# Optimization experiments

Measured on AMD Instinct MI355X. Metric: run time of the kernel, lower is better.

Reference implementation:

```python
import jax, jax.numpy as jnp
import numpy as np

B, C_IN, N, T = 16, 2, 207, 12
E = 1863
EMB = 64
HEADS = 8
F_DIM = EMB * T  # 768


def setup_inputs() -> dict:
    key = jax.random.key(0)
    ks = jax.random.split(key, 12)
    s = 0.05
    x = jax.random.normal(ks[0], (B, C_IN, N, T), jnp.float32)
    src = jax.random.randint(ks[1], (E,), 0, N)
    dst = jax.random.randint(ks[2], (E,), 0, N)
    # ensure every node has an incoming edge (self loops in the tail)
    loop = jnp.arange(N)
    src = src.at[-N:].set(loop)
    dst = dst.at[-N:].set(loop)
    Ws = jax.random.normal(ks[3], (EMB, C_IN), jnp.float32) * s
    bs = jnp.zeros((EMB,), jnp.float32)
    Wc = jax.random.normal(ks[4], (EMB, C_IN), jnp.float32) * s
    bc = jnp.zeros((EMB,), jnp.float32)
    W1 = jax.random.normal(ks[5], (F_DIM, HEADS * F_DIM), jnp.float32) * s
    al1 = jax.random.normal(ks[6], (HEADS, F_DIM), jnp.float32) * s
    ar1 = jax.random.normal(ks[7], (HEADS, F_DIM), jnp.float32) * s
    b1 = jnp.zeros((HEADS, F_DIM), jnp.float32)
    W2 = jax.random.normal(ks[8], (F_DIM, HEADS * F_DIM), jnp.float32) * s
    al2 = jax.random.normal(ks[9], (HEADS, F_DIM), jnp.float32) * s
    ar2 = jax.random.normal(ks[10], (HEADS, F_DIM), jnp.float32) * s
    b2 = jnp.zeros((HEADS, F_DIM), jnp.float32)
    return dict(x=x, src=src, dst=dst, Ws=Ws, bs=bs, Wc=Wc, bc=bc,
                W1=W1, al1=al1, ar1=ar1, b1=b1, W2=W2, al2=al2, ar2=ar2, b2=b2)


def _gat_layer(h, W, al, ar, b, src, dst):
    # h: [B, N, F]  (dropout disabled: eval-mode reference)
    feat = (h @ W).reshape(B, N, HEADS, F_DIM)          # [B,N,H,F]
    el = jnp.einsum('bnhf,hf->bnh', feat, al)           # src scores
    er = jnp.einsum('bnhf,hf->bnh', feat, ar)           # dst scores
    e = jax.nn.leaky_relu(el[:, src] + er[:, dst], 0.2)  # [B,E,H]

    def edge_softmax(ev):  # ev: [E,H], softmax over edges sharing a dst node
        m = jax.ops.segment_max(ev, dst, num_segments=N)
        ex = jnp.exp(ev - m[dst])
        denom = jax.ops.segment_sum(ex, dst, num_segments=N)
        return ex / denom[dst]

    alpha = jax.vmap(edge_softmax)(e)                   # [B,E,H]
    msg = alpha[..., None] * feat[:, src]               # [B,E,H,F]
    rst = jax.vmap(lambda m_: jax.ops.segment_sum(m_, dst, num_segments=N))(msg)
    rst = jax.nn.elu(rst + b)                            # bias + F.elu activation
    return rst.mean(axis=2)                              # mean over heads -> [B,N,F]


def reference(x, src, dst, Ws, bs, Wc, bc, W1, al1, ar1, b1, W2, al2, ar2, b2):
    # 1x1 convs == channel matmuls
    x1 = jnp.einsum('bcnt,oc->bont', x, Ws) + bs[None, :, None, None]
    x2 = jax.nn.leaky_relu(jnp.einsum('bcnt,oc->bont', x, Wc) + bc[None, :, None, None], 0.01)
    xm = x1 + x2                                         # [B,EMB,N,T]
    h = xm.transpose(0, 2, 1, 3).reshape(B, N, F_DIM)    # [B,N,768]
    h = _gat_layer(h, W1, al1, ar1, b1, src, dst)
    h = _gat_layer(h, W2, al2, ar2, b2, src, dst)
    gc = h.reshape(B, N, EMB, T).transpose(0, 2, 1, 3)   # [B,EMB,N,T]
    return xm + gc
```

## Files before the change

### kernel.cpp

```cpp
#include <hip/hip_runtime.h>

#define BB 16
#define NNODE 207
#define TTS 12
#define NE 1863
#define NEP2 1920
#define NH 8
#define FD 768
#define HFD 6144
#define MM 3312
#define MP 3328

typedef short bf16x8 __attribute__((ext_vector_type(8)));
typedef float f32x4 __attribute__((ext_vector_type(4)));

typedef __attribute__((address_space(3))) unsigned int lds_u32;
typedef __attribute__((address_space(1))) const unsigned int glb_u32;

__device__ __forceinline__ unsigned short f2b(float f) {
    unsigned int u = __float_as_uint(f);
    u = (u + 0x7FFFu + ((u >> 16) & 1u)) >> 16;
    return (unsigned short)u;
}
__device__ __forceinline__ float b2f(unsigned short b) {
    return __uint_as_float(((unsigned int)b) << 16);
}

#define CSR_EBLK 468
__global__ __launch_bounds__(256) void prep_misc(const float* __restrict__ W1,
                                                 const float* __restrict__ al1, const float* __restrict__ ar1,
                                                 const float* __restrict__ W2,
                                                 const float* __restrict__ al2, const float* __restrict__ ar2,
                                                 float* __restrict__ wlr,
                                                 unsigned short* __restrict__ Wt1,
                                                 unsigned short* __restrict__ Wt2,
                                                 const int* __restrict__ dst,
                                                 int* __restrict__ ptr, int* __restrict__ cidx) {
    __shared__ __align__(16) char smem[16640];
    const int bid = blockIdx.x;
    const int t = threadIdx.x;
    const int wv = t >> 6, lane = t & 63;
    if (bid < 3072) {
        const int wid = bid * 4 + wv;
        const int which = wid / 6144;
        const int r = wid % 6144;
        const int k = r >> 3, hh = r & 7;
        const float* W = which ? W2 : W1;
        const float* al = which ? al2 : al1;
        const float* ar = which ? ar2 : ar1;
        const float4* wp = (const float4*)(W + (size_t)k * HFD + hh * FD);
        const float4* ap = (const float4*)(al + hh * FD);
        const float4* rp = (const float4*)(ar + hh * FD);
        float sl = 0.f, sr = 0.f;
#pragma unroll
        for (int jj = 0; jj < 3; jj++) {
            int j = lane + jj * 64;
            float4 w = wp[j], a = ap[j], b = rp[j];
            sl += w.x * a.x + w.y * a.y + w.z * a.z + w.w * a.w;
            sr += w.x * b.x + w.y * b.y + w.z * b.z + w.w * b.w;
        }
#pragma unroll
        for (int off = 32; off > 0; off >>= 1) {
            sl += __shfl_down(sl, off);
            sr += __shfl_down(sr, off);
        }
        if (lane == 0) {
            wlr[(size_t)which * 12288 + 0 + hh * FD + k] = sl;
            wlr[(size_t)which * 12288 + 6144 + hh * FD + k] = sr;
        }
    } else if (bid < 5376) {
        float (*tile)[65] = (float(*)[65])smem;
        const int idx = bid - 3072;
        const int which = idx / 1152;
        const int r2 = idx % 1152;
        const int k0 = (r2 % 12) * 64;
        const int n0 = (r2 / 12) * 64;
        const float* W = which ? W2 : W1;
        unsigned short* Wt = which ? Wt2 : Wt1;
        const int c = t & 63, r0 = t >> 6;
#pragma unroll
        for (int i = 0; i < 16; i++) {
            int r = r0 + i * 4;
            tile[r][c] = W[(size_t)(k0 + r) * HFD + n0 + c];
        }
        __syncthreads();
#pragma unroll
        for (int i = 0; i < 16; i++) {
            int r = r0 + i * 4;
            Wt[(size_t)(n0 + r) * FD + k0 + c] = f2b(tile[c][r]);
        }
    } else {
        int* dl = (int*)smem;
        const int b2 = bid - 5376;
        for (int i = t; i < NEP2; i += 256) dl[i] = (i < NE) ? dst[i] : 0x0FFFFFFF;
        __syncthreads();
        if (b2 < CSR_EBLK) {
            const int e = b2 * 4 + wv;
            if (e >= NE) return;
            const int d = dl[e];
            int pos = 0;
#pragma unroll
            for (int j = 0; j < 30; j++) {
                int i = lane + j * 64;
                int di = dl[i];
                pos += (int)(di < d) + (int)((i < e) & (di == d));
            }
#pragma unroll
            for (int off = 32; off > 0; off >>= 1) pos += __shfl_down(pos, off);
            if (lane == 0) cidx[pos] = e;
        } else {
            const int n = (b2 - CSR_EBLK) * 4 + wv;
            if (n > NNODE) return;
            int cnt = 0;
#pragma unroll
            for (int j = 0; j < 30; j++) cnt += (int)(dl[lane + j * 64] < n);
#pragma unroll
            for (int off = 32; off > 0; off >>= 1) cnt += __shfl_down(cnt, off);
            if (lane == 0) ptr[n] = cnt;
        }
    }
}

__global__ __launch_bounds__(256) void prep_h(const float* __restrict__ x,
                                              const float* __restrict__ Ws, const float* __restrict__ bs,
                                              const float* __restrict__ Wc, const float* __restrict__ bc,
                                              const float* __restrict__ wl, const float* __restrict__ wr,
                                              const int* __restrict__ src, const int* __restrict__ cidx,
                                              int* __restrict__ esrc,
                                              float* __restrict__ h0, unsigned short* __restrict__ hbf,
                                              float* __restrict__ el, float* __restrict__ er) {
    __shared__ float redl[4][8], redr[4][8];
    const int bn = blockIdx.x;
    const int t = threadIdx.x;
    if (bn >= MP) {
        int p = (bn - MP) * 256 + t;
        if (p < NE) esrc[p] = src[cidx[p]];
        return;
    }
    if (bn >= MM) {
#pragma unroll
        for (int c = 0; c < 3; c++) hbf[(size_t)bn * FD + c * 256 + t] = 0;
        return;
    }
    const int b = bn / NNODE, n = bn % NNODE;
    float pl[8] = {}, pr[8] = {};
#pragma unroll
    for (int c = 0; c < 3; c++) {
        int idx = c * 256 + t;
        int e = idx / TTS, tt = idx % TTS;
        float x0 = x[((size_t)(b * 2 + 0) * NNODE + n) * TTS + tt];
        float x1 = x[((size_t)(b * 2 + 1) * NNODE + n) * TTS + tt];
        float s1 = Ws[e * 2] * x0 + Ws[e * 2 + 1] * x1 + bs[e];
        float s2 = Wc[e * 2] * x0 + Wc[e * 2 + 1] * x1 + bc[e];
        s2 = s2 > 0.f ? s2 : 0.01f * s2;
        float v = s1 + s2;
        h0[(size_t)bn * FD + idx] = v;
        hbf[(size_t)bn * FD + idx] = f2b(v);
#pragma unroll
        for (int hh = 0; hh < 8; hh++) {
            pl[hh] += v * wl[hh * FD + idx];
            pr[hh] += v * wr[hh * FD + idx];
        }
    }
    const int wv = t >> 6, lane = t & 63;
#pragma unroll
    for (int hh = 0; hh < 8; hh++) {
        float a = pl[hh], c2 = pr[hh];
#pragma unroll
        for (int off = 32; off > 0; off >>= 1) {
            a += __shfl_down(a, off);
            c2 += __shfl_down(c2, off);
        }
        if (lane == 0) { redl[wv][hh] = a; redr[wv][hh] = c2; }
    }
    __syncthreads();
    if (t < 8) {
        el[bn * NH + t] = redl[0][t] + redl[1][t] + redl[2][t] + redl[3][t];
        er[bn * NH + t] = redr[0][t] + redr[1][t] + redr[2][t] + redr[3][t];
    }
}

__global__ __launch_bounds__(256) void gemm_bf16(const unsigned short* __restrict__ A,
                                                 const unsigned short* __restrict__ Bt,
                                                 unsigned short* __restrict__ C) {
    __shared__ __align__(16) unsigned short Alds[128 * 64];
    __shared__ __align__(16) unsigned short Blds[128 * 64];
    const int t = threadIdx.x;
    const int lane = t & 63;
    const int wv = t >> 6;
    const int wr = (wv >> 1) * 64, wc = (wv & 1) * 64;
    const int mt = blockIdx.y * 128, nt = blockIdx.x * 128;
    const int lm = lane & 15;
    const int s4 = lane >> 4;
    const int sl0 = ((0 + s4) ^ (lm & 7)) * 8;
    const int sl1 = ((4 + s4) ^ (lm & 7)) * 8;

    const int rr = lane >> 3;
    const int ssl = ((lane & 7) ^ rr) * 8;
    const unsigned short* ap[4];
    const unsigned short* bp[4];
#pragma unroll
    for (int q = 0; q < 4; q++) {
        int row = wv * 32 + q * 8 + rr;
        ap[q] = A + (size_t)(mt + row) * FD + ssl;
        bp[q] = Bt + (size_t)(nt + row) * FD + ssl;
    }

    f32x4 acc[4][4] = {};
    for (int ks = 0; ks < FD; ks += 64) {
#pragma unroll
        for (int q = 0; q < 4; q++) {
            __builtin_amdgcn_global_load_lds((glb_u32*)(ap[q] + ks),
                (lds_u32*)(Alds + (wv * 4 + q) * 512), 16, 0, 0);
            __builtin_amdgcn_global_load_lds((glb_u32*)(bp[q] + ks),
                (lds_u32*)(Blds + (wv * 4 + q) * 512), 16, 0, 0);
        }
        __syncthreads();
        {
            bf16x8 af[4], bfv[4];
#pragma unroll
            for (int i = 0; i < 4; i++)
                af[i] = *(const bf16x8*)(Alds + (wr + i * 16 + lm) * 64 + sl0);
#pragma unroll
            for (int j = 0; j < 4; j++)
                bfv[j] = *(const bf16x8*)(Blds + (wc + j * 16 + lm) * 64 + sl0);
#pragma unroll
            for (int i = 0; i < 4; i++)
#pragma unroll
                for (int j = 0; j < 4; j++)
                    acc[i][j] = __builtin_amdgcn_mfma_f32_16x16x32_bf16(af[i], bfv[j], acc[i][j], 0, 0, 0);
        }
        {
            bf16x8 af[4], bfv[4];
#pragma unroll
            for (int i = 0; i < 4; i++)
                af[i] = *(const bf16x8*)(Alds + (wr + i * 16 + lm) * 64 + sl1);
#pragma unroll
            for (int j = 0; j < 4; j++)
                bfv[j] = *(const bf16x8*)(Blds + (wc + j * 16 + lm) * 64 + sl1);
#pragma unroll
            for (int i = 0; i < 4; i++)
#pragma unroll
                for (int j = 0; j < 4; j++)
                    acc[i][j] = __builtin_amdgcn_mfma_f32_16x16x32_bf16(af[i], bfv[j], acc[i][j], 0, 0, 0);
        }
        __syncthreads();
    }
    const int rbase = s4 * 4;
#pragma unroll
    for (int i = 0; i < 4; i++) {
#pragma unroll
        for (int r = 0; r < 4; r++) {
            int grow = mt + wr + i * 16 + rbase + r;
            if (grow < MM) {
#pragma unroll
                for (int j = 0; j < 4; j++) {
                    int gcol = nt + wc + j * 16 + lm;
                    C[(size_t)grow * HFD + gcol] = f2b(acc[i][j][r]);
                }
            }
        }
    }
}

template <int LAST>
__global__ __launch_bounds__(512) void msg_agg(const unsigned short* __restrict__ feat,
                                               const int* __restrict__ cptr, const int* __restrict__ esrc,
                                               const float* __restrict__ bias,
                                               const float* __restrict__ el_in, const float* __restrict__ er_in,
                                               unsigned short* __restrict__ hbf_out,
                                               const float* __restrict__ wl, const float* __restrict__ wr,
                                               float* __restrict__ el_out, float* __restrict__ er_out,
                                               const float* __restrict__ h0, float* __restrict__ out) {
    __shared__ float rstl[HFD];
    __shared__ int src_l[64];
    __shared__ float alph[64][NH];
    __shared__ float redl[8][8], redr[8][8];
    __shared__ float sm_m[8], sm_i[8], sm_er[8];
    const int bn = (blockIdx.x & 7) * (MM / 8) + (blockIdx.x >> 3);
    const int b = bn / NNODE, n = bn % NNODE;
    const int t = threadIdx.x;
    const int p0 = cptr[n], p1 = cptr[n + 1];
    const int deg = p1 - p0;
    if (t < 64) {
        const int h = t & 7, js = t >> 3;
        const float erv = er_in[(b * NNODE + n) * NH + h];
        float m = -1e30f, d = 0.f;
        for (int jb = 0; jb < deg; jb += 8) {
            int j = jb + js;
            float s = -1e30f, add = 0.f;
            if (j < deg) {
                int sn = esrc[p0 + j];
                s = el_in[(b * NNODE + sn) * NH + h] + erv;
                s = s > 0.f ? s : 0.2f * s;
                add = 1.f;
            }
            float mn = fmaxf(m, s);
            d = d * __expf(m - mn) + add * __expf(s - mn);
            m = mn;
        }
#pragma unroll
        for (int o = 8; o < 64; o <<= 1) {
            float mo = __shfl_xor(m, o), dd = __shfl_xor(d, o);
            float mn = fmaxf(m, mo);
            d = d * __expf(m - mn) + dd * __expf(mo - mn);
            m = mn;
        }
        if (js == 0) { sm_m[h] = m; sm_i[h] = 1.f / d; sm_er[h] = erv; }
    }
    __syncthreads();

    const int hq0 = (0 * 512 + t) / 192;
    const int hq1 = (1 * 512 + t) / 192;
    const int hq2 = (2 * 512 + t) / 192;
    float acc[3][4] = {};
    for (int base = p0; base < p1; base += 64) {
        const int cnt = min(64, p1 - base);
        if (t < cnt) src_l[t] = esrc[base + t];
        {
            int j = t >> 3, hh = t & 7;
            if (j < cnt) {
                float s = el_in[(b * NNODE + esrc[base + j]) * NH + hh] + sm_er[hh];
                s = s > 0.f ? s : 0.2f * s;
                alph[j][hh] = __expf(s - sm_m[hh]) * sm_i[hh];
            }
        }
        __syncthreads();
        for (int j2 = 0; j2 < cnt; j2++) {
            const uint2* fp = (const uint2*)(feat + (size_t)(b * NNODE + src_l[j2]) * HFD);
            const float a0 = alph[j2][hq0], a1 = alph[j2][hq1], a2 = alph[j2][hq2];
            uint2 v0 = fp[0 * 512 + t], v1 = fp[1 * 512 + t], v2 = fp[2 * 512 + t];
            unsigned int w;
            w = v0.x; acc[0][0] += a0 * b2f((unsigned short)w); acc[0][1] += a0 * b2f((unsigned short)(w >> 16));
            w = v0.y; acc[0][2] += a0 * b2f((unsigned short)w); acc[0][3] += a0 * b2f((unsigned short)(w >> 16));
            w = v1.x; acc[1][0] += a1 * b2f((unsigned short)w); acc[1][1] += a1 * b2f((unsigned short)(w >> 16));
            w = v1.y; acc[1][2] += a1 * b2f((unsigned short)w); acc[1][3] += a1 * b2f((unsigned short)(w >> 16));
            w = v2.x; acc[2][0] += a2 * b2f((unsigned short)w); acc[2][1] += a2 * b2f((unsigned short)(w >> 16));
            w = v2.y; acc[2][2] += a2 * b2f((unsigned short)w); acc[2][3] += a2 * b2f((unsigned short)(w >> 16));
        }
        __syncthreads();
    }
#pragma unroll
    for (int q = 0; q < 3; q++) {
        int s = q * 512 + t;
#pragma unroll
        for (int u = 0; u < 4; u++) rstl[s * 4 + u] = acc[q][u];
    }
    __syncthreads();
    float pl[8] = {}, pr[8] = {};
#pragma unroll
    for (int q2 = 0; q2 < 2; q2++) {
        int f = q2 * 512 + t;
        if (f < FD) {
            float val = 0.f;
#pragma unroll
            for (int hh = 0; hh < 8; hh++) {
                float r = rstl[hh * FD + f] + bias[hh * FD + f];
                val += (r > 0.f) ? r : (expf(r) - 1.f);
            }
            val *= 0.125f;
            if (LAST) {
                int e_ = f / TTS, tt_ = f % TTS;
                out[((size_t)(b * 64 + e_) * NNODE + n) * TTS + tt_] = h0[(size_t)bn * FD + f] + val;
            } else {
                hbf_out[(size_t)bn * FD + f] = f2b(val);
#pragma unroll
                for (int hh = 0; hh < 8; hh++) {
                    pl[hh] += val * wl[hh * FD + f];
                    pr[hh] += val * wr[hh * FD + f];
                }
            }
        }
    }
    if (!LAST) {
        const int wv = t >> 6, lane = t & 63;
#pragma unroll
        for (int hh = 0; hh < 8; hh++) {
            float a = pl[hh], c2 = pr[hh];
#pragma unroll
            for (int off = 32; off > 0; off >>= 1) {
                a += __shfl_down(a, off);
                c2 += __shfl_down(c2, off);
            }
            if (lane == 0) { redl[wv][hh] = a; redr[wv][hh] = c2; }
        }
        __syncthreads();
        if (t < 8) {
            float a = 0.f, c2 = 0.f;
#pragma unroll
            for (int wv2 = 0; wv2 < 8; wv2++) { a += redl[wv2][t]; c2 += redr[wv2][t]; }
            el_out[bn * NH + t] = a;
            er_out[bn * NH + t] = c2;
        }
    }
}

extern "C" void kernel_launch(void* const* d_in, const int* in_sizes, int n_in,
                              void* d_out, int out_size, void* d_ws, size_t ws_size,
                              hipStream_t stream) {
    const float* x = (const float*)d_in[0];
    const int* src = (const int*)d_in[1];
    const int* dst = (const int*)d_in[2];
    const float* Ws = (const float*)d_in[3];
    const float* bs = (const float*)d_in[4];
    const float* Wc = (const float*)d_in[5];
    const float* bc = (const float*)d_in[6];
    const float* W1 = (const float*)d_in[7];
    const float* al1 = (const float*)d_in[8];
    const float* ar1 = (const float*)d_in[9];
    const float* b1 = (const float*)d_in[10];
    const float* W2 = (const float*)d_in[11];
    const float* al2 = (const float*)d_in[12];
    const float* ar2 = (const float*)d_in[13];
    const float* b2 = (const float*)d_in[14];
    float* out = (float*)d_out;

    char* w = (char*)d_ws;
    size_t off = 0;
    auto alloc = [&](size_t bytes) -> void* {
        void* p = w + off;
        off = (off + bytes + 255) & ~(size_t)255;
        return p;
    };
    float* h0 = (float*)alloc((size_t)MM * FD * 4);
    unsigned short* hbf = (unsigned short*)alloc((size_t)MP * FD * 2);
    unsigned short* Wt1 = (unsigned short*)alloc((size_t)HFD * FD * 2);
    unsigned short* Wt2 = (unsigned short*)alloc((size_t)HFD * FD * 2);
    unsigned short* feat = (unsigned short*)alloc((size_t)MM * HFD * 2);
    float* el = (float*)alloc((size_t)MM * NH * 4);
    float* er = (float*)alloc((size_t)MM * NH * 4);
    float* el2 = (float*)alloc((size_t)MM * NH * 4);
    float* er2 = (float*)alloc((size_t)MM * NH * 4);
    int* cptr = (int*)alloc((NNODE + 1) * 4);
    int* cidx = (int*)alloc(NE * 4);
    int* esrc = (int*)alloc(NE * 4);
    float* wlr = (float*)alloc((size_t)4 * 6144 * 4);
    float* wl1 = wlr, * wr1 = wlr + 6144, * wl2 = wlr + 12288, * wr2 = wlr + 18432;

    prep_misc<<<5896, 256, 0, stream>>>(W1, al1, ar1, W2, al2, ar2, wlr, Wt1, Wt2, dst, cptr, cidx);
    prep_h<<<MP + 8, 256, 0, stream>>>(x, Ws, bs, Wc, bc, wl1, wr1, src, cidx, esrc, h0, hbf, el, er);

    gemm_bf16<<<dim3(48, 26), 256, 0, stream>>>(hbf, Wt1, feat);
    msg_agg<0><<<MM, 512, 0, stream>>>(feat, cptr, esrc, b1, el, er, hbf, wl2, wr2, el2, er2, nullptr, nullptr);

    gemm_bf16<<<dim3(48, 26), 256, 0, stream>>>(hbf, Wt2, feat);
    msg_agg<1><<<MM, 512, 0, stream>>>(feat, cptr, esrc, b2, el2, er2, nullptr, nullptr, nullptr, nullptr, nullptr, h0, out);
}
```

Before: 215.1 us.

## Halve msg_agg block size, widen feature loads, prefetch next edge's row

The message-aggregation kernel now runs 256 threads per block instead of 512. Each thread loads 16-byte vectors, eight bf16 features at a time, and accumulates 3x8 values. While the current edge is being accumulated, the next edge's source feature row is loaded into registers, so gather latency overlaps with the FMAs. Edge chunks and the wave-reduction arrays shrink to match. In exchange, register pressure per thread rises and there are fewer threads per node to hide latency.

```diff
diff --git a/kernel.cpp b/kernel.cpp
--- a/kernel.cpp
+++ b/kernel.cpp
@@ -264,7 +264,7 @@
 }
 
 template <int LAST>
-__global__ __launch_bounds__(512) void msg_agg(const unsigned short* __restrict__ feat,
+__global__ __launch_bounds__(256) void msg_agg(const unsigned short* __restrict__ feat,
                                                const int* __restrict__ cptr, const int* __restrict__ esrc,
                                                const float* __restrict__ bias,
                                                const float* __restrict__ el_in, const float* __restrict__ er_in,
@@ -273,9 +273,9 @@
                                                float* __restrict__ el_out, float* __restrict__ er_out,
                                                const float* __restrict__ h0, float* __restrict__ out) {
     __shared__ float rstl[HFD];
-    __shared__ int src_l[64];
-    __shared__ float alph[64][NH];
-    __shared__ float redl[8][8], redr[8][8];
+    __shared__ int src_l[32];
+    __shared__ float alph[32][NH];
+    __shared__ float redl[4][8], redr[4][8];
     __shared__ float sm_m[8], sm_i[8], sm_er[8];
     const int bn = (blockIdx.x & 7) * (MM / 8) + (blockIdx.x >> 3);
     const int b = bn / NNODE, n = bn % NNODE;
@@ -310,12 +310,10 @@
     }
     __syncthreads();
 
-    const int hq0 = (0 * 512 + t) / 192;
-    const int hq1 = (1 * 512 + t) / 192;
-    const int hq2 = (2 * 512 + t) / 192;
-    float acc[3][4] = {};
-    for (int base = p0; base < p1; base += 64) {
-        const int cnt = min(64, p1 - base);
+    const int h0i = t / 96, h1i = (256 + t) / 96, h2i = (512 + t) / 96;
+    float acc[3][8] = {};
+    for (int base = p0; base < p1; base += 32) {
+        const int cnt = min(32, p1 - base);
         if (t < cnt) src_l[t] = esrc[base + t];
         {
             int j = t >> 3, hh = t & 7;
@@ -326,49 +324,63 @@
             }
         }
         __syncthreads();
+        const unsigned short* fp = feat + (size_t)(b * NNODE + src_l[0]) * HFD;
+        uint4 c0 = *(const uint4*)(fp + (size_t)(0 * 256 + t) * 8);
+        uint4 c1 = *(const uint4*)(fp + (size_t)(1 * 256 + t) * 8);
+        uint4 c2 = *(const uint4*)(fp + (size_t)(2 * 256 + t) * 8);
         for (int j2 = 0; j2 < cnt; j2++) {
-            const uint2* fp = (const uint2*)(feat + (size_t)(b * NNODE + src_l[j2]) * HFD);
-            const float a0 = alph[j2][hq0], a1 = alph[j2][hq1], a2 = alph[j2][hq2];
-            uint2 v0 = fp[0 * 512 + t], v1 = fp[1 * 512 + t], v2 = fp[2 * 512 + t];
+            uint4 n0, n1, n2;
+            if (j2 + 1 < cnt) {
+                const unsigned short* np = feat + (size_t)(b * NNODE + src_l[j2 + 1]) * HFD;
+                n0 = *(const uint4*)(np + (size_t)(0 * 256 + t) * 8);
+                n1 = *(const uint4*)(np + (size_t)(1 * 256 + t) * 8);
+                n2 = *(const uint4*)(np + (size_t)(2 * 256 + t) * 8);
+            }
+            const float a0 = alph[j2][h0i], a1 = alph[j2][h1i], a2 = alph[j2][h2i];
             unsigned int w;
-            w = v0.x; acc[0][0] += a0 * b2f((unsigned short)w); acc[0][1] += a0 * b2f((unsigned short)(w >> 16));
-            w = v0.y; acc[0][2] += a0 * b2f((unsigned short)w); acc[0][3] += a0 * b2f((unsigned short)(w >> 16));
-            w = v1.x; acc[1][0] += a1 * b2f((unsigned short)w); acc[1][1] += a1 * b2f((unsigned short)(w >> 16));
-            w = v1.y; acc[1][2] += a1 * b2f((unsigned short)w); acc[1][3] += a1 * b2f((unsigned short)(w >> 16));
-            w = v2.x; acc[2][0] += a2 * b2f((unsigned short)w); acc[2][1] += a2 * b2f((unsigned short)(w >> 16));
-            w = v2.y; acc[2][2] += a2 * b2f((unsigned short)w); acc[2][3] += a2 * b2f((unsigned short)(w >> 16));
-        }
-        __syncthreads();
-    }
-#pragma unroll
-    for (int q = 0; q < 3; q++) {
-        int s = q * 512 + t;
-#pragma unroll
-        for (int u = 0; u < 4; u++) rstl[s * 4 + u] = acc[q][u];
+            w = c0.x; acc[0][0] += a0 * b2f((unsigned short)w); acc[0][1] += a0 * b2f((unsigned short)(w >> 16));
+            w = c0.y; acc[0][2] += a0 * b2f((unsigned short)w); acc[0][3] += a0 * b2f((unsigned short)(w >> 16));
+            w = c0.z; acc[0][4] += a0 * b2f((unsigned short)w); acc[0][5] += a0 * b2f((unsigned short)(w >> 16));
+            w = c0.w; acc[0][6] += a0 * b2f((unsigned short)w); acc[0][7] += a0 * b2f((unsigned short)(w >> 16));
+            w = c1.x; acc[1][0] += a1 * b2f((unsigned short)w); acc[1][1] += a1 * b2f((unsigned short)(w >> 16));
+            w = c1.y; acc[1][2] += a1 * b2f((unsigned short)w); acc[1][3] += a1 * b2f((unsigned short)(w >> 16));
+            w = c1.z; acc[1][4] += a1 * b2f((unsigned short)w); acc[1][5] += a1 * b2f((unsigned short)(w >> 16));
+            w = c1.w; acc[1][6] += a1 * b2f((unsigned short)w); acc[1][7] += a1 * b2f((unsigned short)(w >> 16));
+            w = c2.x; acc[2][0] += a2 * b2f((unsigned short)w); acc[2][1] += a2 * b2f((unsigned short)(w >> 16));
+            w = c2.y; acc[2][2] += a2 * b2f((unsigned short)w); acc[2][3] += a2 * b2f((unsigned short)(w >> 16));
+            w = c2.z; acc[2][4] += a2 * b2f((unsigned short)w); acc[2][5] += a2 * b2f((unsigned short)(w >> 16));
+            w = c2.w; acc[2][6] += a2 * b2f((unsigned short)w); acc[2][7] += a2 * b2f((unsigned short)(w >> 16));
+            c0 = n0; c1 = n1; c2 = n2;
+        }
+        __syncthreads();
+    }
+#pragma unroll
+    for (int c = 0; c < 3; c++) {
+        int v = c * 256 + t;
+#pragma unroll
+        for (int u = 0; u < 8; u++) rstl[v * 8 + u] = acc[c][u];
     }
     __syncthreads();
     float pl[8] = {}, pr[8] = {};
 #pragma unroll
-    for (int q2 = 0; q2 < 2; q2++) {
-        int f = q2 * 512 + t;
-        if (f < FD) {
-            float val = 0.f;
+    for (int q = 0; q < 3; q++) {
+        int f = q * 256 + t;
+        float val = 0.f;
+#pragma unroll
+        for (int hh = 0; hh < 8; hh++) {
+            float r = rstl[hh * FD + f] + bias[hh * FD + f];
+            val += (r > 0.f) ? r : (expf(r) - 1.f);
+        }
+        val *= 0.125f;
+        if (LAST) {
+            int e_ = f / TTS, tt_ = f % TTS;
+            out[((size_t)(b * 64 + e_) * NNODE + n) * TTS + tt_] = h0[(size_t)bn * FD + f] + val;
+        } else {
+            hbf_out[(size_t)bn * FD + f] = f2b(val);
 #pragma unroll
             for (int hh = 0; hh < 8; hh++) {
-                float r = rstl[hh * FD + f] + bias[hh * FD + f];
-                val += (r > 0.f) ? r : (expf(r) - 1.f);
-            }
-            val *= 0.125f;
-            if (LAST) {
-                int e_ = f / TTS, tt_ = f % TTS;
-                out[((size_t)(b * 64 + e_) * NNODE + n) * TTS + tt_] = h0[(size_t)bn * FD + f] + val;
-            } else {
-                hbf_out[(size_t)bn * FD + f] = f2b(val);
-#pragma unroll
-                for (int hh = 0; hh < 8; hh++) {
-                    pl[hh] += val * wl[hh * FD + f];
-                    pr[hh] += val * wr[hh * FD + f];
-                }
+                pl[hh] += val * wl[hh * FD + f];
+                pr[hh] += val * wr[hh * FD + f];
             }
         }
     }
@@ -386,11 +398,8 @@
         }
         __syncthreads();
         if (t < 8) {
-            float a = 0.f, c2 = 0.f;
-#pragma unroll
-            for (int wv2 = 0; wv2 < 8; wv2++) { a += redl[wv2][t]; c2 += redr[wv2][t]; }
-            el_out[bn * NH + t] = a;
-            er_out[bn * NH + t] = c2;
+            el_out[bn * NH + t] = redl[0][t] + redl[1][t] + redl[2][t] + redl[3][t];
+            er_out[bn * NH + t] = redr[0][t] + redr[1][t] + redr[2][t] + redr[3][t];
         }
     }
 }
@@ -441,8 +450,8 @@
     prep_h<<<MP + 8, 256, 0, stream>>>(x, Ws, bs, Wc, bc, wl1, wr1, src, cidx, esrc, h0, hbf, el, er);
 
     gemm_bf16<<<dim3(48, 26), 256, 0, stream>>>(hbf, Wt1, feat);
-    msg_agg<0><<<MM, 512, 0, stream>>>(feat, cptr, esrc, b1, el, er, hbf, wl2, wr2, el2, er2, nullptr, nullptr);
+    msg_agg<0><<<MM, 256, 0, stream>>>(feat, cptr, esrc, b1, el, er, hbf, wl2, wr2, el2, er2, nullptr, nullptr);
 
     gemm_bf16<<<dim3(48, 26), 256, 0, stream>>>(hbf, Wt2, feat);
-    msg_agg<1><<<MM, 512, 0, stream>>>(feat, cptr, esrc, b2, el2, er2, nullptr, nullptr, nullptr, nullptr, nullptr, h0, out);
-}
+    msg_agg<1><<<MM, 256, 0, stream>>>(feat, cptr, esrc, b2, el2, er2, nullptr, nullptr, nullptr, nullptr, nullptr, h0, out);
+}
```

Result: faster. 200.7 us (-6.7%).
